# Performance work log

Hardware: AMD Instinct MI355X
Metric: run time of the kernel (lower is better)

The kernel has to match this reference:

```python
import jax, jax.numpy as jnp
import numpy as np

NUM_BANDS = 8
WINDOW = 2048
OVERLAP = 1024
SR = 16000


def _band_mask(L):
    # Replicates torch: band = searchsorted(band_ranges, |freq|, left) - 1.
    # DC bin gives band=-1 which torch negative-indexes into the LAST band,
    # hence the mod. All bins satisfy band < NUM_BANDS, so all are assigned.
    freqs = np.fft.fftfreq(L, 1.0 / SR)
    ranges = np.linspace(0.0, SR / 2.0, NUM_BANDS + 1)
    idx = np.searchsorted(ranges, np.abs(freqs), side='left') - 1
    idx = idx % NUM_BANDS
    mask = (idx[None, :] == np.arange(NUM_BANDS)[:, None]).astype(np.float32)
    return jnp.asarray(mask)  # [bands, L]


def _band_signals(x):
    # mag*exp(i*phase) of masked bins == masked complex bins; ifft().real per band
    L = x.shape[-1]
    X = jnp.fft.fft(x)                         # [B, L] complex
    mask = _band_mask(L)                       # [bands, L]
    Xb = X[:, None, :] * mask[None, :, :]      # [B, bands, L]
    return jnp.fft.ifft(Xb).real               # [B, bands, L]


def _chunks(sig):
    L = sig.shape[-1]
    hop = WINDOW - OVERLAP
    n = (L - OVERLAP) // hop                   # num_chunks (static)
    idx = (jnp.arange(n) * hop)[:, None] + jnp.arange(WINDOW)[None, :]  # [n, W]
    return sig[:, :, idx]                       # [B, bands, n, W]


def _loudness(x):
    # BS.1770-style energy loudness (vectorized stand-in for the repo's
    # undefined `loudness` helper): -0.691 + 10*log10(mean square)
    ms = jnp.mean(x * x, axis=-1)
    return -0.691 + 10.0 * jnp.log10(ms + 1e-12)


def reference(watermarked_signals, original_signals):
    ro = _band_signals(original_signals)
    rw = _band_signals(watermarked_signals)
    lo = _loudness(_chunks(ro))                # [B, bands, n]
    lw = _loudness(_chunks(rw))
    lo = jnp.where(jnp.isnan(lo), 0.0, lo)
    lw = jnp.where(jnp.isnan(lw), 0.0, lw)
    diff = (lw - lo).reshape(-1)               # ordered (i, j, k) like the torch loop
    w = jax.nn.softmax(diff)
    return jnp.sum(w * diff)


def setup_inputs() -> dict:
    key = jax.random.key(0)
    k1, k2 = jax.random.split(key)
    B, L = 8, 160000
    return {
        'watermarked_signals': jax.random.normal(k1, (B, L), dtype=jnp.float32),
        'original_signals': jax.random.normal(k2, (B, L), dtype=jnp.float32),
    }
```

## Files before the change

kernel.cpp:

```cpp
#include <hip/hip_runtime.h>
#include <hip/hip_fp16.h>
#include <math.h>

constexpr int L      = 160000;
constexpr int BATCH  = 8;
constexpr int NB     = 8;
constexpr int NHOPS  = 156;
constexpr int NCHUNK = 155;
constexpr int RS     = 289;
constexpr float TWO_PI = 6.28318530717958647692f;
constexpr float INVL = 1.0f / (float)L;

__device__ __forceinline__ float2 cmulf(float2 a, float2 b) {
  return make_float2(a.x * b.x - a.y * b.y, a.x * b.y + a.y * b.x);
}

__device__ __forceinline__ float2 cisf(float a) {
  float s, c;
  __sincosf(a, &s, &c);
  return make_float2(c, s);
}

__device__ __forceinline__ int pad8(int i) { return i + (i >> 3); }

template <int SIGN>
__device__ __forceinline__ void bf4s(float2* v) {
  float2 t0 = make_float2(v[0].x + v[2].x, v[0].y + v[2].y);
  float2 t1 = make_float2(v[0].x - v[2].x, v[0].y - v[2].y);
  float2 t2 = make_float2(v[1].x + v[3].x, v[1].y + v[3].y);
  float2 t3 = make_float2(v[1].x - v[3].x, v[1].y - v[3].y);
  v[0] = make_float2(t0.x + t2.x, t0.y + t2.y);
  v[2] = make_float2(t0.x - t2.x, t0.y - t2.y);
  if constexpr (SIGN < 0) {
    v[1] = make_float2(t1.x + t3.y, t1.y - t3.x);
    v[3] = make_float2(t1.x - t3.y, t1.y + t3.x);
  } else {
    v[1] = make_float2(t1.x - t3.y, t1.y + t3.x);
    v[3] = make_float2(t1.x + t3.y, t1.y - t3.x);
  }
}

template <int SIGN>
__device__ __forceinline__ void bf5s(float2* v) {
  const float c1 = 0.30901699437494745f, s1 = 0.9510565162951535f;
  const float c2 = -0.8090169943749475f, s2 = 0.5877852522924731f;
  float2 t1 = make_float2(v[1].x + v[4].x, v[1].y + v[4].y);
  float2 t3 = make_float2(v[1].x - v[4].x, v[1].y - v[4].y);
  float2 t2 = make_float2(v[2].x + v[3].x, v[2].y + v[3].y);
  float2 t4 = make_float2(v[2].x - v[3].x, v[2].y - v[3].y);
  float2 a = make_float2(v[0].x + c1 * t1.x + c2 * t2.x, v[0].y + c1 * t1.y + c2 * t2.y);
  float2 b = make_float2(s1 * t3.x + s2 * t4.x, s1 * t3.y + s2 * t4.y);
  float2 c = make_float2(v[0].x + c2 * t1.x + c1 * t2.x, v[0].y + c2 * t1.y + c1 * t2.y);
  float2 d = make_float2(s2 * t3.x - s1 * t4.x, s2 * t3.y - s1 * t4.y);
  v[0] = make_float2(v[0].x + t1.x + t2.x, v[0].y + t1.y + t2.y);
  if constexpr (SIGN < 0) {
    v[1] = make_float2(a.x + b.y, a.y - b.x);
    v[4] = make_float2(a.x - b.y, a.y + b.x);
    v[2] = make_float2(c.x + d.y, c.y - d.x);
    v[3] = make_float2(c.x - d.y, c.y + d.x);
  } else {
    v[1] = make_float2(a.x - b.y, a.y + b.x);
    v[4] = make_float2(a.x + b.y, a.y - b.x);
    v[2] = make_float2(c.x - d.y, c.y + d.x);
    v[3] = make_float2(c.x + d.y, c.y - d.x);
  }
}

template <int R>
__device__ __forceinline__ void twchain(float2* v, float2 t1) {
  float2 t = t1;
  v[1] = cmulf(v[1], t);
#pragma unroll
  for (int r = 2; r < R; ++r) { t = cmulf(t, t1); v[r] = cmulf(v[r], t); }
}

__device__ __forceinline__ int rev3_5(int q) {
  int q5 = q / 5, q25 = q / 25;
  int d0 = q - 5 * q5, d1 = q5 - 5 * q25;
  return 25 * d0 + 5 * d1 + q25;
}

__device__ __forceinline__ int rev3_4(int q) {
  return ((q & 3) << 4) | (q & 12) | (q >> 4);
}

template <int SUB, int SIGN>
__device__ __forceinline__ void dif5_ip_stage_c(float2* a, int ln) {
  int i1 = ln, i2 = ln + 64;
  bool g2 = (i2 < 125);
  int j1 = i1 % SUB, j2 = i2 % SUB;
  int b1 = (i1 / SUB) * (5 * SUB) + j1;
  int b2 = (i2 / SUB) * (5 * SUB) + j2;
  float2 u[5], v[5];
#pragma unroll
  for (int r = 0; r < 5; ++r) u[r] = a[b1 + SUB * r];
  if (g2) {
#pragma unroll
    for (int r = 0; r < 5; ++r) v[r] = a[b2 + SUB * r];
  }
  bf5s<SIGN>(u);
  twchain<5>(u, cisf((float)SIGN * (TWO_PI / (float)(5 * SUB)) * (float)j1));
  if (g2) {
    bf5s<SIGN>(v);
    twchain<5>(v, cisf((float)SIGN * (TWO_PI / (float)(5 * SUB)) * (float)j2));
  }
#pragma unroll
  for (int r = 0; r < 5; ++r) a[b1 + SUB * r] = u[r];
  if (g2) {
#pragma unroll
    for (int r = 0; r < 5; ++r) a[b2 + SUB * r] = v[r];
  }
}

template <int SUB>
__device__ __forceinline__ void dif5_ip_stage_t(float2* a, int ln, float2 t1a, float2 t1b) {
  int i1 = ln, i2 = ln + 64;
  bool g2 = (i2 < 125);
  int j1 = i1 % SUB, j2 = i2 % SUB;
  int b1 = (i1 / SUB) * (5 * SUB) + j1;
  int b2 = (i2 / SUB) * (5 * SUB) + j2;
  float2 u[5], v[5];
#pragma unroll
  for (int r = 0; r < 5; ++r) u[r] = a[b1 + SUB * r];
  if (g2) {
#pragma unroll
    for (int r = 0; r < 5; ++r) v[r] = a[b2 + SUB * r];
  }
  bf5s<1>(u);
  twchain<5>(u, t1a);
  if (g2) {
    bf5s<1>(v);
    twchain<5>(v, t1b);
  }
#pragma unroll
  for (int r = 0; r < 5; ++r) a[b1 + SUB * r] = u[r];
  if (g2) {
#pragma unroll
    for (int r = 0; r < 5; ++r) a[b2 + SUB * r] = v[r];
  }
}

template <int SIGN>
__device__ __forceinline__ void dif625_ip(float2* a, int ln) {
  dif5_ip_stage_c<125, SIGN>(a, ln);
  dif5_ip_stage_c<25, SIGN>(a, ln);
  dif5_ip_stage_c<5, SIGN>(a, ln);
  int q1 = ln, q2 = ln + 64;
  bool g2 = (q2 < 125);
  float2 u[5], v[5];
#pragma unroll
  for (int r = 0; r < 5; ++r) u[r] = a[5 * q1 + r];
  if (g2) {
#pragma unroll
    for (int r = 0; r < 5; ++r) v[r] = a[5 * q2 + r];
  }
  bf5s<SIGN>(u);
  if (g2) bf5s<SIGN>(v);
  int rv1 = rev3_5(q1), rv2 = rev3_5(q2);
#pragma unroll
  for (int r = 0; r < 5; ++r) a[125 * r + rv1] = u[r];
  if (g2) {
#pragma unroll
    for (int r = 0; r < 5; ++r) a[125 * r + rv2] = v[r];
  }
}

template <int SIGN>
__device__ __forceinline__ void dif256sw_ip(float2* a, int ln) {
  {
    float2 u[4];
#pragma unroll
    for (int r = 0; r < 4; ++r) u[r] = a[pad8(ln + 64 * r)];
    bf4s<SIGN>(u);
    twchain<4>(u, cisf((float)SIGN * (TWO_PI / 256.0f) * (float)ln));
#pragma unroll
    for (int r = 0; r < 4; ++r) a[pad8(ln + 64 * r)] = u[r];
  }
  {
    int j = ln & 15, b = 64 * (ln >> 4) + j;
    float2 u[4];
#pragma unroll
    for (int r = 0; r < 4; ++r) u[r] = a[pad8(b + 16 * r)];
    bf4s<SIGN>(u);
    twchain<4>(u, cisf((float)SIGN * (TWO_PI / 64.0f) * (float)j));
#pragma unroll
    for (int r = 0; r < 4; ++r) a[pad8(b + 16 * r)] = u[r];
  }
  {
    int j = ln & 3, b = 16 * (ln >> 2) + j;
    float2 u[4];
#pragma unroll
    for (int r = 0; r < 4; ++r) u[r] = a[pad8(b + 4 * r)];
    bf4s<SIGN>(u);
    twchain<4>(u, cisf((float)SIGN * (TWO_PI / 16.0f) * (float)j));
#pragma unroll
    for (int r = 0; r < 4; ++r) a[pad8(b + 4 * r)] = u[r];
  }
  {
    float2 u[4];
#pragma unroll
    for (int r = 0; r < 4; ++r) u[r] = a[pad8(4 * ln + r)];
    bf4s<SIGN>(u);
    int rv = rev3_4(ln);
#pragma unroll
    for (int r = 0; r < 4; ++r) a[pad8(64 * r + rv)] = u[r];
  }
}

__global__ __launch_bounds__(256) void f1_kernel(const float* __restrict__ win,
                                                 const float* __restrict__ oin,
                                                 float2* __restrict__ G,
                                                 float* __restrict__ E) {
  __shared__ float2 A[4 * 625];
  int blk = blockIdx.x;
  int gid = blk * 256 + threadIdx.x;
  if (gid < 2 * BATCH * NB * NHOPS) E[gid] = 0.0f;
  int sig = blk >> 6, g = blk & 63;
  int n1base = g * 4;
  int tid = threadIdx.x;
  const float4* wp4 = (const float4*)(win + (size_t)sig * L);
  const float4* op4 = (const float4*)(oin + (size_t)sig * L);
  for (int r = tid; r < 625; r += 256) {
    float4 wv = wp4[r * 64 + g];
    float4 ov = op4[r * 64 + g];
    A[0 * 625 + r] = make_float2(wv.x, ov.x);
    A[1 * 625 + r] = make_float2(wv.y, ov.y);
    A[2 * 625 + r] = make_float2(wv.z, ov.z);
    A[3 * 625 + r] = make_float2(wv.w, ov.w);
  }
  __syncthreads();
  int wv_ = tid >> 6, ln = tid & 63;
  dif625_ip<-1>(A + wv_ * 625, ln);
  __syncthreads();
  int cc = tid & 3, k20 = tid >> 2;
  int n1 = n1base + cc;
  float w = -(TWO_PI / (float)L) * (float)n1;
  float2 t = cisf(w * (float)k20);
  float2 stp = cisf(w * 64.0f);
  for (int k2 = k20; k2 < 625; k2 += 64) {
    G[(size_t)sig * L + k2 * 256 + n1] = cmulf(A[cc * 625 + k2], t);
    t = cmulf(t, stp);
  }
}

__global__ __launch_bounds__(1024) void fi_kernel(const float2* __restrict__ G,
                                                  __half2* __restrict__ H) {
  __shared__ float2 Xb[16 * RS];
  __shared__ float2 Wb[16 * RS];
  int blk = blockIdx.x;
  int bg  = blk / (BATCH * 40);
  int rem = blk - bg * (BATCH * 40);
  int sig = rem / 40, gr = rem % 40;
  int k2base = gr * 16;
  int tid = threadIdx.x;
  int wv = tid >> 6, ln = tid & 63;
  int k2 = k2base + wv;
  bool act = (k2 < 625);
  float2* xr = Xb + wv * RS;
  float2* wr = Wb + wv * RS;
  if (act) {
#pragma unroll
    for (int r = 0; r < 4; ++r)
      xr[pad8(ln + 64 * r)] = G[(size_t)sig * L + k2 * 256 + ln + 64 * r];
    dif256sw_ip<-1>(xr, ln);
  }
  int cc = tid & 15, n1g = tid >> 4;
  int k2e = k2base + cc;
  float a0 = (TWO_PI / (float)L) * (float)k2e;
  float2 t0 = cisf(a0 * (float)n1g);
  float2 stp = cisf(a0 * 64.0f);
  float2 zero = make_float2(0.0f, 0.0f);

#pragma unroll
  for (int bi = 0; bi < 2; ++bi) {
    int band = bg * 2 + bi;
    int lo1, hi1, lo2, hi2;
    if (band < 7) {
      lo1 = 10000 * band + 1;        hi1 = 10000 * (band + 1);
      lo2 = L - 10000 * (band + 1);  hi2 = L - 10000 * band - 1;
    } else {
      lo1 = 70001; hi1 = 80000; lo2 = 80001; hi2 = 89999;
    }
    if (act) {
      for (int k1 = ln; k1 < 256; k1 += 64) wr[pad8(k1)] = zero;
      int s1 = (lo1 - k2 + 624) / 625;
      int e1 = (hi1 - k2) / 625; if (e1 > 255) e1 = 255;
      int s2 = (lo2 - k2 + 624) / 625;
      int e2 = (hi2 - k2) / 625; if (e2 > 255) e2 = 255;
      int c1 = e1 - s1 + 1;
      int c2 = e2 - s2 + 1;
      if (ln < c1) { int k1 = s1 + ln; wr[pad8(k1)] = xr[pad8(k1)]; }
      int l2 = ln - 32;
      if (l2 >= 0 && l2 < c2) { int k1 = s2 + l2; wr[pad8(k1)] = xr[pad8(k1)]; }
      if (band == 7 && k2 == 0 && ln == 0) wr[pad8(0)] = xr[pad8(0)];
      dif256sw_ip<1>(wr, ln);
    }
    __syncthreads();
    if (k2e < 625) {
      size_t obase = (size_t)(sig * NB + band) * L;
      float2 t = t0;
#pragma unroll
      for (int it = 0; it < 4; ++it) {
        int n1 = n1g + 64 * it;
        float2 val = cmulf(Wb[cc * RS + pad8(n1)], t);
        H[obase + (size_t)n1 * 625 + k2e] = __floats2half2_rn(val.x * INVL, val.y * INVL);
        t = cmulf(t, stp);
      }
    }
    __syncthreads();
  }
}

__global__ __launch_bounds__(256) void i2_kernel(const __half2* __restrict__ H,
                                                 float* __restrict__ E) {
  __shared__ float2 A[4 * 625];
  __shared__ float P[4 * 2 * NHOPS];
  int blk = blockIdx.x;
  int g = blk & 31, sb = blk >> 5;
  int band = sb & 7, sig = sb >> 3;
  int tid = threadIdx.x;
  int wv = tid >> 6, ln = tid & 63;
  size_t base = (size_t)(sig * NB + band) * L;
  int n1A = 8 * g + wv, n1B = 8 * g + 4 + wv;
  const __half2* HA = H + base + (size_t)n1A * 625;
  const __half2* HB = H + base + (size_t)n1B * 625;
  int j1 = ln, j2 = ln + 64;
  bool g2 = (j2 < 125);
  __half2 hA1[5], hA2[5], hB1[5], hB2[5];
#pragma unroll
  for (int r = 0; r < 5; ++r) hA1[r] = HA[j1 + 125 * r];
  if (g2) {
#pragma unroll
    for (int r = 0; r < 5; ++r) hA2[r] = HA[j2 + 125 * r];
  }
#pragma unroll
  for (int r = 0; r < 5; ++r) hB1[r] = HB[j1 + 125 * r];
  if (g2) {
#pragma unroll
    for (int r = 0; r < 5; ++r) hB2[r] = HB[j2 + 125 * r];
  }
  float2 tS1a = cisf((TWO_PI / 625.0f) * (float)j1);
  float2 tS1b = cisf((TWO_PI / 625.0f) * (float)j2);
  float2 tS2a = cisf((TWO_PI / 125.0f) * (float)(j1 % 25));
  float2 tS2b = cisf((TWO_PI / 125.0f) * (float)(j2 % 25));
  float2 tS3a = cisf((TWO_PI / 25.0f) * (float)(j1 % 5));
  float2 tS3b = cisf((TWO_PI / 25.0f) * (float)(j2 % 5));
  float2* a = A + wv * 625;
  float* Pw = P + wv * (2 * NHOPS);

  {
    float2 u[5];
#pragma unroll
    for (int r = 0; r < 5; ++r) u[r] = __half22float2(hA1[r]);
    bf5s<1>(u);
    twchain<5>(u, tS1a);
#pragma unroll
    for (int r = 0; r < 5; ++r) a[j1 + 125 * r] = u[r];
    if (g2) {
      float2 v[5];
#pragma unroll
      for (int r = 0; r < 5; ++r) v[r] = __half22float2(hA2[r]);
      bf5s<1>(v);
      twchain<5>(v, tS1b);
#pragma unroll
      for (int r = 0; r < 5; ++r) a[j2 + 125 * r] = v[r];
    }
  }
  dif5_ip_stage_t<25>(a, ln, tS2a, tS2b);
  dif5_ip_stage_t<5>(a, ln, tS3a, tS3b);
  {
    float2 u[5], v[5];
#pragma unroll
    for (int r = 0; r < 5; ++r) u[r] = a[5 * j1 + r];
    if (g2) {
#pragma unroll
      for (int r = 0; r < 5; ++r) v[r] = a[5 * j2 + r];
    }
    bf5s<1>(u);
    if (g2) bf5s<1>(v);
    int rv1 = rev3_5(j1), rv2 = rev3_5(j2);
#pragma unroll
    for (int r = 0; r < 5; ++r) a[125 * r + rv1] = u[r];
    if (g2) {
#pragma unroll
      for (int r = 0; r < 5; ++r) a[125 * r + rv2] = v[r];
    }
  }
  for (int h = ln; h < NHOPS; h += 64) {
    float ex = 0.0f, ey = 0.0f;
#pragma unroll
    for (int d = 0; d < 4; ++d) {
      float2 z = a[4 * h + d];
      ex += z.x * z.x;
      ey += z.y * z.y;
    }
    Pw[h] = ex;
    Pw[NHOPS + h] = ey;
  }

  {
    float2 u[5];
#pragma unroll
    for (int r = 0; r < 5; ++r) u[r] = __half22float2(hB1[r]);
    bf5s<1>(u);
    twchain<5>(u, tS1a);
#pragma unroll
    for (int r = 0; r < 5; ++r) a[j1 + 125 * r] = u[r];
    if (g2) {
      float2 v[5];
#pragma unroll
      for (int r = 0; r < 5; ++r) v[r] = __half22float2(hB2[r]);
      bf5s<1>(v);
      twchain<5>(v, tS1b);
#pragma unroll
      for (int r = 0; r < 5; ++r) a[j2 + 125 * r] = v[r];
    }
  }
  dif5_ip_stage_t<25>(a, ln, tS2a, tS2b);
  dif5_ip_stage_t<5>(a, ln, tS3a, tS3b);
  {
    float2 u[5], v[5];
#pragma unroll
    for (int r = 0; r < 5; ++r) u[r] = a[5 * j1 + r];
    if (g2) {
#pragma unroll
      for (int r = 0; r < 5; ++r) v[r] = a[5 * j2 + r];
    }
    bf5s<1>(u);
    if (g2) bf5s<1>(v);
    int rv1 = rev3_5(j1), rv2 = rev3_5(j2);
#pragma unroll
    for (int r = 0; r < 5; ++r) a[125 * r + rv1] = u[r];
    if (g2) {
#pragma unroll
      for (int r = 0; r < 5; ++r) a[125 * r + rv2] = v[r];
    }
  }
  for (int h = ln; h < NHOPS; h += 64) {
    float ex = 0.0f, ey = 0.0f;
#pragma unroll
    for (int d = 0; d < 4; ++d) {
      float2 z = a[4 * h + d];
      ex += z.x * z.x;
      ey += z.y * z.y;
    }
    Pw[h] += ex;
    Pw[NHOPS + h] += ey;
  }
  __syncthreads();
  int eb = (sig * NB + band) * NHOPS;
  for (int idx = tid; idx < 2 * NHOPS; idx += 256) {
    float v = P[idx] + P[2 * NHOPS + idx] + P[4 * NHOPS + idx] + P[6 * NHOPS + idx];
    int comp = idx / NHOPS, h = idx - comp * NHOPS;
    atomicAdd(&E[comp * (BATCH * NB * NHOPS) + eb + h], v);
  }
}

__global__ __launch_bounds__(1024) void finalize_kernel(const float* __restrict__ E,
                                                        float* __restrict__ out) {
  constexpr int ND = BATCH * NB * NCHUNK;
  constexpr float SC = 1.0f / 2048.0f;
  __shared__ float diffs[ND];
  __shared__ float sred[1024];
  int tid = threadIdx.x;
  for (int idx = tid; idx < ND; idx += 1024) {
    int sb = idx / NCHUNK;
    int k = idx - sb * NCHUNK;
    float msw = (E[sb * NHOPS + k] + E[sb * NHOPS + k + 1]) * SC;
    float mso = (E[64 * NHOPS + sb * NHOPS + k] + E[64 * NHOPS + sb * NHOPS + k + 1]) * SC;
    float lw = -0.691f + 10.0f * log10f(msw + 1e-12f);
    float lo = -0.691f + 10.0f * log10f(mso + 1e-12f);
    diffs[idx] = lw - lo;
  }
  __syncthreads();
  float mx = -3.4e38f;
  for (int idx = tid; idx < ND; idx += 1024) mx = fmaxf(mx, diffs[idx]);
  sred[tid] = mx;
  __syncthreads();
  for (int s = 512; s > 0; s >>= 1) {
    if (tid < s) sred[tid] = fmaxf(sred[tid], sred[tid + s]);
    __syncthreads();
  }
  float gmax = sred[0];
  __syncthreads();
  float se = 0.0f, swd = 0.0f;
  for (int idx = tid; idx < ND; idx += 1024) {
    float d = diffs[idx];
    float e = expf(d - gmax);
    se += e;
    swd += d * e;
  }
  sred[tid] = se; __syncthreads();
  for (int s = 512; s > 0; s >>= 1) { if (tid < s) sred[tid] += sred[tid + s]; __syncthreads(); }
  float tot = sred[0];
  __syncthreads();
  sred[tid] = swd; __syncthreads();
  for (int s = 512; s > 0; s >>= 1) { if (tid < s) sred[tid] += sred[tid + s]; __syncthreads(); }
  if (tid == 0) out[0] = sred[0] / tot;
}

extern "C" void kernel_launch(void* const* d_in, const int* in_sizes, int n_in,
                              void* d_out, int out_size, void* d_ws, size_t ws_size,
                              hipStream_t stream) {
  (void)in_sizes; (void)n_in; (void)out_size; (void)ws_size;
  char* ws = (char*)d_ws;
  float2*  G = (float2*)ws;
  __half2* H = (__half2*)(ws + 10240000);
  float*   E = (float*)(ws + 51200000);
  const float* w = (const float*)d_in[0];
  const float* o = (const float*)d_in[1];

  f1_kernel<<<dim3(BATCH * 64), dim3(256), 0, stream>>>(w, o, G, E);
  fi_kernel<<<dim3(4 * BATCH * 40), dim3(1024), 0, stream>>>(G, H);
  i2_kernel<<<dim3(BATCH * NB * 32), dim3(256), 0, stream>>>(H, E);
  finalize_kernel<<<dim3(1), dim3(1024), 0, stream>>>(E, (float*)d_out);
}
```

Before: 158.3 us.

## Fuse band masking and last FFT stage into fi_kernel, hoist twiddles

Precomputes the per-lane 256-point FFT twiddles once per thread instead of evaluating sincos in every stage call. The band mask is applied in registers while loading the first stage, which removes the separate zeroing pass and the conditional copies. The final radix-4 stage of the inverse transform now runs inside the output-writing threads instead of a separate in-place pass. This removes shared-memory round trips and transcendental work, but the band-7 range logic and the bit-reversed output indexing had to be rewritten, so correctness depends on that index arithmetic.

```diff
diff --git a/kernel.cpp b/kernel.cpp
--- a/kernel.cpp
+++ b/kernel.cpp
@@ -20,6 +20,8 @@
   __sincosf(a, &s, &c);
   return make_float2(c, s);
 }
+
+__device__ __forceinline__ float2 conjf(float2 a) { return make_float2(a.x, -a.y); }
 
 __device__ __forceinline__ int pad8(int i) { return i + (i >> 3); }
 
@@ -166,35 +168,37 @@
 }
 
 template <int SIGN>
-__device__ __forceinline__ void dif256sw_ip(float2* a, int ln) {
-  {
+__device__ __forceinline__ void dif256sw_tw(float2* a, int ln,
+                                            float2 tw1, float2 tw2, float2 tw3) {
+  {
+    int b = pad8(ln);
     float2 u[4];
 #pragma unroll
-    for (int r = 0; r < 4; ++r) u[r] = a[pad8(ln + 64 * r)];
+    for (int r = 0; r < 4; ++r) u[r] = a[b + 72 * r];
     bf4s<SIGN>(u);
-    twchain<4>(u, cisf((float)SIGN * (TWO_PI / 256.0f) * (float)ln));
-#pragma unroll
-    for (int r = 0; r < 4; ++r) a[pad8(ln + 64 * r)] = u[r];
-  }
-  {
-    int j = ln & 15, b = 64 * (ln >> 4) + j;
+    twchain<4>(u, tw1);
+#pragma unroll
+    for (int r = 0; r < 4; ++r) a[b + 72 * r] = u[r];
+  }
+  {
+    int j = ln & 15, b = pad8(64 * (ln >> 4) + j);
     float2 u[4];
 #pragma unroll
-    for (int r = 0; r < 4; ++r) u[r] = a[pad8(b + 16 * r)];
+    for (int r = 0; r < 4; ++r) u[r] = a[b + 18 * r];
     bf4s<SIGN>(u);
-    twchain<4>(u, cisf((float)SIGN * (TWO_PI / 64.0f) * (float)j));
-#pragma unroll
-    for (int r = 0; r < 4; ++r) a[pad8(b + 16 * r)] = u[r];
-  }
-  {
-    int j = ln & 3, b = 16 * (ln >> 2) + j;
+    twchain<4>(u, tw2);
+#pragma unroll
+    for (int r = 0; r < 4; ++r) a[b + 18 * r] = u[r];
+  }
+  {
+    int j = ln & 3, jb = 16 * (ln >> 2) + j;
     float2 u[4];
 #pragma unroll
-    for (int r = 0; r < 4; ++r) u[r] = a[pad8(b + 4 * r)];
+    for (int r = 0; r < 4; ++r) u[r] = a[pad8(jb + 4 * r)];
     bf4s<SIGN>(u);
-    twchain<4>(u, cisf((float)SIGN * (TWO_PI / 16.0f) * (float)j));
-#pragma unroll
-    for (int r = 0; r < 4; ++r) a[pad8(b + 4 * r)] = u[r];
+    twchain<4>(u, tw3);
+#pragma unroll
+    for (int r = 0; r < 4; ++r) a[pad8(jb + 4 * r)] = u[r];
   }
   {
     float2 u[4];
@@ -258,51 +262,81 @@
   bool act = (k2 < 625);
   float2* xr = Xb + wv * RS;
   float2* wr = Wb + wv * RS;
+
+  float2 tw1 = cisf((TWO_PI / 256.0f) * (float)ln);
+  float2 tw2 = cisf((TWO_PI / 64.0f) * (float)(ln & 15));
+  float2 tw3 = cisf((TWO_PI / 16.0f) * (float)(ln & 3));
+
   if (act) {
 #pragma unroll
     for (int r = 0; r < 4; ++r)
       xr[pad8(ln + 64 * r)] = G[(size_t)sig * L + k2 * 256 + ln + 64 * r];
-    dif256sw_ip<-1>(xr, ln);
-  }
-  int cc = tid & 15, n1g = tid >> 4;
+    dif256sw_tw<-1>(xr, ln, conjf(tw1), conjf(tw2), conjf(tw3));
+  }
+
+  int b1 = pad8(ln);
+  int b2 = pad8(64 * (ln >> 4) + (ln & 15));
+  int jb3 = 16 * (ln >> 2) + (ln & 3);
+  int kb = 625 * ln + k2;
+
+  int cc = tid & 15, q = tid >> 4;
+  int rq = rev3_4(q);
   int k2e = k2base + cc;
+  bool eact = (k2e < 625);
   float a0 = (TWO_PI / (float)L) * (float)k2e;
-  float2 t0 = cisf(a0 * (float)n1g);
+  float2 t0q = cisf(a0 * (float)rq);
   float2 stp = cisf(a0 * 64.0f);
-  float2 zero = make_float2(0.0f, 0.0f);
+  int b4 = cc * RS + pad8(4 * q);
 
 #pragma unroll
   for (int bi = 0; bi < 2; ++bi) {
     int band = bg * 2 + bi;
-    int lo1, hi1, lo2, hi2;
+    unsigned lo1, d1, lo2, d2;
     if (band < 7) {
-      lo1 = 10000 * band + 1;        hi1 = 10000 * (band + 1);
-      lo2 = L - 10000 * (band + 1);  hi2 = L - 10000 * band - 1;
+      lo1 = 10000u * band + 1u;              d1 = 9999u;
+      lo2 = (unsigned)L - 10000u * (band + 1); d2 = 9999u;
     } else {
-      lo1 = 70001; hi1 = 80000; lo2 = 80001; hi2 = 89999;
+      lo1 = 70001u; d1 = 19998u;
+      lo2 = 0u;     d2 = 0u;
     }
     if (act) {
-      for (int k1 = ln; k1 < 256; k1 += 64) wr[pad8(k1)] = zero;
-      int s1 = (lo1 - k2 + 624) / 625;
-      int e1 = (hi1 - k2) / 625; if (e1 > 255) e1 = 255;
-      int s2 = (lo2 - k2 + 624) / 625;
-      int e2 = (hi2 - k2) / 625; if (e2 > 255) e2 = 255;
-      int c1 = e1 - s1 + 1;
-      int c2 = e2 - s2 + 1;
-      if (ln < c1) { int k1 = s1 + ln; wr[pad8(k1)] = xr[pad8(k1)]; }
-      int l2 = ln - 32;
-      if (l2 >= 0 && l2 < c2) { int k1 = s2 + l2; wr[pad8(k1)] = xr[pad8(k1)]; }
-      if (band == 7 && k2 == 0 && ln == 0) wr[pad8(0)] = xr[pad8(0)];
-      dif256sw_ip<1>(wr, ln);
+      float2 u[4];
+#pragma unroll
+      for (int r = 0; r < 4; ++r) {
+        float2 x = xr[b1 + 72 * r];
+        unsigned k = (unsigned)(kb + 40000 * r);
+        bool in = ((k - lo1) <= d1) || ((k - lo2) <= d2);
+        u[r] = in ? x : make_float2(0.0f, 0.0f);
+      }
+      bf4s<1>(u);
+      twchain<4>(u, tw1);
+#pragma unroll
+      for (int r = 0; r < 4; ++r) wr[b1 + 72 * r] = u[r];
+#pragma unroll
+      for (int r = 0; r < 4; ++r) u[r] = wr[b2 + 18 * r];
+      bf4s<1>(u);
+      twchain<4>(u, tw2);
+#pragma unroll
+      for (int r = 0; r < 4; ++r) wr[b2 + 18 * r] = u[r];
+#pragma unroll
+      for (int r = 0; r < 4; ++r) u[r] = wr[pad8(jb3 + 4 * r)];
+      bf4s<1>(u);
+      twchain<4>(u, tw3);
+#pragma unroll
+      for (int r = 0; r < 4; ++r) wr[pad8(jb3 + 4 * r)] = u[r];
     }
     __syncthreads();
-    if (k2e < 625) {
+    if (eact) {
       size_t obase = (size_t)(sig * NB + band) * L;
-      float2 t = t0;
-#pragma unroll
-      for (int it = 0; it < 4; ++it) {
-        int n1 = n1g + 64 * it;
-        float2 val = cmulf(Wb[cc * RS + pad8(n1)], t);
+      float2 v[4];
+#pragma unroll
+      for (int r = 0; r < 4; ++r) v[r] = Wb[b4 + r];
+      bf4s<1>(v);
+      float2 t = t0q;
+#pragma unroll
+      for (int r = 0; r < 4; ++r) {
+        int n1 = 64 * r + rq;
+        float2 val = cmulf(v[r], t);
         H[obase + (size_t)n1 * 625 + k2e] = __floats2half2_rn(val.x * INVL, val.y * INVL);
         t = cmulf(t, stp);
       }
```

New measurement: 144.1 us. 1.1x faster.
